# Optimization experiments

Measured on AMD Instinct MI355X. Metric: run time of the kernel, lower is better.

The kernel has to match this reference:

```python
import jax, jax.numpy as jnp
import numpy as np

N, D, E = 50000, 128, 800000
EPS_BN = 1e-5
EPS_NORM = 1e-12


def setup_inputs() -> dict:
    key = jax.random.key(0)
    ks = jax.random.split(key, 12)
    s = 1.0 / np.sqrt(D)  # xavier-ish scale for [D,D] weights
    return {
        "x": jax.random.normal(ks[0], (N, D), jnp.float32),
        "perb": jax.random.normal(ks[1], (N, D), jnp.float32) * 0.05,
        "edge_row": jax.random.randint(ks[2], (E,), 0, N, jnp.int32),
        "edge_col": jax.random.randint(ks[3], (E,), 0, N, jnp.int32),
        "edge_w": jax.random.uniform(ks[4], (E,), jnp.float32),
        "W_on": jax.random.normal(ks[5], (D, D), jnp.float32) * s,
        "b_on": jnp.zeros((D,), jnp.float32),
        "W_tg": jax.random.normal(ks[6], (D, D), jnp.float32) * s,
        "b_tg": jnp.zeros((D,), jnp.float32),
        "W1": jax.random.normal(ks[7], (D, D), jnp.float32) * s,
        "b1": jnp.zeros((D,), jnp.float32),
        "bn_g": jnp.ones((D,), jnp.float32),
        "bn_b": jnp.zeros((D,), jnp.float32),
        "prelu_a": jnp.full((1,), 0.25, jnp.float32),
        "W2": jax.random.normal(ks[8], (D, D), jnp.float32) * s,
        "b2": jnp.zeros((D,), jnp.float32),
    }


def _gcn(x, W, b, row, col, w):
    # dense matmul then sparse aggregation: out = A @ (x W) + b
    h = x @ W                              # [N, D]
    msg = h[col] * w[:, None]              # gather + edge weight, [E, D]
    agg = jax.ops.segment_sum(msg, row, num_segments=N)  # scatter-add, [N, D]
    return agg + b


def _predictor(x, W1, b1, g, beta, a, W2, b2):
    h = x @ W1 + b1
    mu = h.mean(axis=0)
    var = h.var(axis=0)  # biased, as torch BatchNorm1d normalization
    h = (h - mu) / jnp.sqrt(var + EPS_BN) * g + beta
    h = jnp.where(h > 0, h, a * h)  # PReLU (single shared slope)
    return h @ W2 + b2


def _l2norm(x):
    n = jnp.sqrt(jnp.sum(x * x, axis=-1, keepdims=True))
    return x / jnp.maximum(n, EPS_NORM)


def _loss_fn(x, y):
    return 2.0 - 2.0 * jnp.sum(_l2norm(x) * _l2norm(y), axis=-1)


def reference(x, perb, edge_row, edge_col, edge_w,
              W_on, b_on, W_tg, b_tg,
              W1, b1, bn_g, bn_b, prelu_a, W2, b2):
    x2 = x + perb
    embed = x2 + _gcn(x2, W_on, b_on, edge_row, edge_col, edge_w)
    online_x = _gcn(x, W_on, b_on, edge_row, edge_col, edge_w)
    online_y = _gcn(x2, W_on, b_on, edge_row, edge_col, edge_w)
    target_y = jax.lax.stop_gradient(_gcn(x, W_tg, b_tg, edge_row, edge_col, edge_w))
    target_x = jax.lax.stop_gradient(_gcn(x2, W_tg, b_tg, edge_row, edge_col, edge_w))
    px = _predictor(online_x, W1, b1, bn_g, bn_b, prelu_a, W2, b2)
    py = _predictor(online_y, W1, b1, bn_g, bn_b, prelu_a, W2, b2)
    loss = (_loss_fn(px, target_x) + _loss_fn(py, target_y)).mean()
    return embed, loss
```

## Files before the change

### kernel.cpp

```cpp
#include <hip/hip_runtime.h>

typedef unsigned int u32;
typedef unsigned short u16;
typedef __attribute__((ext_vector_type(8))) short short8;
typedef __attribute__((ext_vector_type(4))) float floatx4;

union F8 { uint4 u4; short8 s8; };

#define CAP 64
#define CSTR 16

__device__ __forceinline__ float bf2f(u32 lo16) { return __uint_as_float(lo16 << 16); }
__device__ __forceinline__ u16 f2bf(float f) {
    u32 u = __float_as_uint(f);
    return (u16)((u + 0x7FFFu + ((u >> 16) & 1u)) >> 16);
}
__device__ __forceinline__ u32 pack2(float a, float b) {
    return (u32)f2bf(a) | ((u32)f2bf(b) << 16);
}

__global__ __launch_bounds__(256) void k_front(
    const float* __restrict__ x, const float* __restrict__ perb,
    const int* __restrict__ erow, const int* __restrict__ ecol, const float* __restrict__ ew,
    const float* __restrict__ Won, const float* __restrict__ Wtg,
    const float* __restrict__ W1, const float* __restrict__ W2,
    const float* __restrict__ b_on, const float* __restrict__ b1,
    u16* __restrict__ XS, int* __restrict__ cnt, u32* __restrict__ cpack,
    u16* __restrict__ Wfrag, float* __restrict__ c1,
    int N, int E, int NC, int NS)
{
    int b = blockIdx.x, t = threadIdx.x;
    if (b < 8) {
        int s = (b << 8) + t;
        int lane = s & 63;
        int n = ((s >> 8) << 4) + (lane & 15);
        int k0 = ((s >> 6) & 3) * 32 + (lane >> 4) * 8;
        float v[8];
#pragma unroll
        for (int jj = 0; jj < 8; jj++) v[jj] = 0.f;
        for (int m2 = 0; m2 < 128; m2++) {
            float w1v = W1[m2 * 128 + n];
#pragma unroll
            for (int jj = 0; jj < 8; jj++)
                v[jj] = fmaf(Won[(k0 + jj) * 128 + m2], w1v, v[jj]);
        }
        ((uint4*)(Wfrag + 2 * 16384))[s] =
            make_uint4(pack2(v[0], v[1]), pack2(v[2], v[3]), pack2(v[4], v[5]), pack2(v[6], v[7]));
    } else if (b == 8) {
        if (t < 128) {
            float s = b1[t];
            for (int k = 0; k < 128; k++) s = fmaf(b_on[k], W1[k * 128 + t], s);
            c1[t] = s;
        }
    } else if (b < 12) {
        const float* W = (b == 9) ? Won : (b == 10 ? Wtg : W2);
        int mi = (b == 9) ? 0 : (b == 10 ? 1 : 3);
        uint4* out = (uint4*)(Wfrag + (size_t)mi * 16384);
        for (int s = t; s < 2048; s += 256) {
            int lane = s & 63;
            int n = ((s >> 8) << 4) + (lane & 15);
            int k0 = ((s >> 6) & 3) * 32 + (lane >> 4) * 8;
            u32 p[4];
#pragma unroll
            for (int jj = 0; jj < 4; jj++) {
                float a = W[(size_t)(k0 + 2 * jj) * 128 + n];
                float bb = W[(size_t)(k0 + 2 * jj + 1) * 128 + n];
                p[jj] = pack2(a, bb);
            }
            out[s] = make_uint4(p[0], p[1], p[2], p[3]);
        }
    } else {
        int t2 = b - 12;
        int T = NC + NS;
        int sc_before = (int)(((long long)t2 * NC) / T);
        int sc_after  = (int)(((long long)(t2 + 1) * NC) / T);
        if (sc_after > sc_before) {
            int e = sc_before * 256 + t;
            if (e < E) {
                int r = erow[e];
                u32 wq = (u32)__float2uint_rn(ew[e] * 65536.f);
                if (wq > 65535u) wq = 65535u;
                u32 rec = (u32)ecol[e] | (wq << 16);
                int tk = atomicAdd(&cnt[r * CSTR], 1);
                if (tk < CAP) cpack[(size_t)r * CAP + tk] = rec;
            }
        } else {
            int tid = (t2 - sc_before) * 256 + t;
            if (tid < N * 32) {
                int row = tid >> 5, seg = tid & 31;
                float4 xv = *(const float4*)(x + (size_t)row * 128 + seg * 4);
                float4 pv = *(const float4*)(perb + (size_t)row * 128 + seg * 4);
                u16* r = XS + (size_t)row * 256 + seg * 4;
                *(uint2*)r = make_uint2(pack2(xv.x, xv.y), pack2(xv.z, xv.w));
                *(uint2*)(r + 128) = make_uint2(pack2(xv.x + pv.x, xv.y + pv.y), pack2(xv.z + pv.z, xv.w + pv.w));
            }
        }
    }
}

__global__ __launch_bounds__(256) void k_agg(
    const u16* __restrict__ XS, const int* __restrict__ cnt,
    const u32* __restrict__ cpack, u16* __restrict__ AG, int N)
{
    int wave = threadIdx.x >> 6, lane = threadIdx.x & 63;
    int node = blockIdx.x * 4 + wave;
    if (node >= N) return;
    int d = cnt[node * CSTR];
    if (d > CAP) d = CAP;
    const u32* seg = cpack + (size_t)node * CAP;
    float a0 = 0.f, a1 = 0.f, a2 = 0.f, a3 = 0.f;
#pragma unroll 4
    for (int e = 0; e < d; e++) {
        u32 rec = seg[e];
        int c = (int)(rec & 0xffffu);
        float w = (float)(rec >> 16) * (1.f / 65536.f);
        uint2 v = ((const uint2*)(XS + (size_t)c * 256))[lane];
        a0 = fmaf(w, bf2f(v.x & 0xffffu), a0);
        a1 = fmaf(w, bf2f(v.x >> 16), a1);
        a2 = fmaf(w, bf2f(v.y & 0xffffu), a2);
        a3 = fmaf(w, bf2f(v.y >> 16), a3);
    }
    ((uint2*)(AG + (size_t)node * 256))[lane] = make_uint2(pack2(a0, a1), pack2(a2, a3));
}

__global__ __launch_bounds__(512) void k_hemb(
    const u16* __restrict__ AG, const u16* __restrict__ Wfrag,
    const float* __restrict__ c1, const float* __restrict__ b_on,
    const u16* __restrict__ XS,
    u16* __restrict__ h1x, u16* __restrict__ h1y, float* __restrict__ out,
    int N, int ntiles)
{
    __shared__ uint4 sW[4096];
    const int wave = threadIdx.x >> 6, lane = threadIdx.x & 63;
    const int m = lane & 15, q = lane >> 4;
    const uint4* wfWon = (const uint4*)Wfrag;
    const uint4* wfWc  = (const uint4*)(Wfrag + 2 * 16384);
#pragma unroll
    for (int i = threadIdx.x; i < 2048; i += 512) {
        sW[i]        = wfWon[i];
        sW[i + 2048] = wfWc[i];
    }
    __syncthreads();
    for (int tile = blockIdx.x; tile < ntiles; tile += gridDim.x) {
        const int grow = tile * 128 + wave * 16 + m;
        const int rc = grow < N ? grow : N - 1;
        const bool valid = grow < N;
        const u16* ar = AG + (size_t)rc * 256;
        short8 fa[4], fb[4];
#pragma unroll
        for (int ks = 0; ks < 4; ks++) {
            int c0 = ks * 32 + q * 8;
            F8 t;
            t.u4 = *(const uint4*)(ar + c0);       fa[ks] = t.s8;
            t.u4 = *(const uint4*)(ar + 128 + c0); fb[ks] = t.s8;
        }
#pragma unroll 2
        for (int ct = 0; ct < 8; ct++) {
            floatx4 ax = {0.f, 0.f, 0.f, 0.f}, ay = {0.f, 0.f, 0.f, 0.f}, em = {0.f, 0.f, 0.f, 0.f};
#pragma unroll
            for (int ks = 0; ks < 4; ks++) {
                F8 wc, wo;
                wo.u4 = sW[(ct * 4 + ks) * 64 + lane];
                wc.u4 = sW[2048 + (ct * 4 + ks) * 64 + lane];
                ax = __builtin_amdgcn_mfma_f32_16x16x32_bf16(wc.s8, fa[ks], ax, 0, 0, 0);
                ay = __builtin_amdgcn_mfma_f32_16x16x32_bf16(wc.s8, fb[ks], ay, 0, 0, 0);
                em = __builtin_amdgcn_mfma_f32_16x16x32_bf16(wo.s8, fb[ks], em, 0, 0, 0);
            }
            if (valid) {
                int c0 = ct * 16 + q * 4;
                float4 cv = *(const float4*)(c1 + c0);
                float4 bo = *(const float4*)(b_on + c0);
                uint2 xs2 = *(const uint2*)(XS + (size_t)grow * 256 + 128 + c0);
                *(uint2*)(h1x + (size_t)grow * 128 + c0) =
                    make_uint2(pack2(ax[0] + cv.x, ax[1] + cv.y), pack2(ax[2] + cv.z, ax[3] + cv.w));
                *(uint2*)(h1y + (size_t)grow * 128 + c0) =
                    make_uint2(pack2(ay[0] + cv.x, ay[1] + cv.y), pack2(ay[2] + cv.z, ay[3] + cv.w));
                float4 o;
                o.x = bf2f(xs2.x & 0xffffu) + em[0] + bo.x;
                o.y = bf2f(xs2.x >> 16)     + em[1] + bo.y;
                o.z = bf2f(xs2.y & 0xffffu) + em[2] + bo.z;
                o.w = bf2f(xs2.y >> 16)     + em[3] + bo.w;
                *(float4*)(out + (size_t)grow * 128 + c0) = o;
            }
        }
    }
}

__global__ __launch_bounds__(256) void k_bnstats(
    const u32* __restrict__ h1x32, const u32* __restrict__ h1y32,
    float* __restrict__ sums, int* __restrict__ tick,
    const float* __restrict__ g, const float* __restrict__ beta,
    float* __restrict__ bnp, int N)
{
    int c2 = threadIdx.x & 63, gg = threadIdx.x >> 6;
    int per = (N + gridDim.x - 1) / gridDim.x;
    int r0 = blockIdx.x * per, r1 = r0 + per;
    if (r1 > N) r1 = N;
    float s[8] = {0.f, 0.f, 0.f, 0.f, 0.f, 0.f, 0.f, 0.f};
    for (int r = r0 + gg; r < r1; r += 4) {
        u32 vx = h1x32[(size_t)r * 64 + c2];
        float lo = bf2f(vx & 0xffffu), hi = bf2f(vx >> 16);
        s[0] += lo; s[1] = fmaf(lo, lo, s[1]); s[2] += hi; s[3] = fmaf(hi, hi, s[3]);
        u32 vy = h1y32[(size_t)r * 64 + c2];
        lo = bf2f(vy & 0xffffu); hi = bf2f(vy >> 16);
        s[4] += lo; s[5] = fmaf(lo, lo, s[5]); s[6] += hi; s[7] = fmaf(hi, hi, s[7]);
    }
    __shared__ float red[256][8];
    __shared__ int lastflag;
#pragma unroll
    for (int k = 0; k < 8; k++) red[threadIdx.x][k] = s[k];
    __syncthreads();
    if (gg == 0) {
        float v[8];
#pragma unroll
        for (int k = 0; k < 8; k++)
            v[k] = red[c2][k] + red[c2 + 64][k] + red[c2 + 128][k] + red[c2 + 192][k];
        int c0 = 2 * c2, c1i = c0 + 1;
        atomicAdd(&sums[c0], v[0]);        atomicAdd(&sums[128 + c0], v[1]);
        atomicAdd(&sums[c1i], v[2]);       atomicAdd(&sums[128 + c1i], v[3]);
        atomicAdd(&sums[256 + c0], v[4]);  atomicAdd(&sums[384 + c0], v[5]);
        atomicAdd(&sums[256 + c1i], v[6]); atomicAdd(&sums[384 + c1i], v[7]);
    }
    __syncthreads();
    if (threadIdx.x == 0) {
        __threadfence();
        int old = atomicAdd(tick, 1);
        lastflag = (old == (int)gridDim.x - 1) ? 1 : 0;
    }
    __syncthreads();
    if (lastflag && threadIdx.x < 128) {
        int d = threadIdx.x;
        float inv = 1.0f / (float)N;
        float s0 = atomicAdd(&sums[d], 0.f);
        float s1 = atomicAdd(&sums[128 + d], 0.f);
        float s2 = atomicAdd(&sums[256 + d], 0.f);
        float s3 = atomicAdd(&sums[384 + d], 0.f);
        float mux = s0 * inv;
        float varx = s1 * inv - mux * mux;
        float isx = rsqrtf(varx + 1e-5f);
        bnp[d]       = g[d] * isx;
        bnp[128 + d] = beta[d] - mux * g[d] * isx;
        float muy = s2 * inv;
        float vary = s3 * inv - muy * muy;
        float isy = rsqrtf(vary + 1e-5f);
        bnp[256 + d] = g[d] * isy;
        bnp[384 + d] = beta[d] - muy * g[d] * isy;
    }
}

__device__ __forceinline__ short8 bn_frag(const u16* hrow, const float* sc, const float* sh,
                                          int c0, float slope) {
    uint4 h = *(const uint4*)(hrow + c0);
    float4 s0 = *(const float4*)(sc + c0), s1 = *(const float4*)(sc + c0 + 4);
    float4 t0 = *(const float4*)(sh + c0), t1 = *(const float4*)(sh + c0 + 4);
    float v[8];
    v[0] = fmaf(bf2f(h.x & 0xffffu), s0.x, t0.x);
    v[1] = fmaf(bf2f(h.x >> 16),     s0.y, t0.y);
    v[2] = fmaf(bf2f(h.y & 0xffffu), s0.z, t0.z);
    v[3] = fmaf(bf2f(h.y >> 16),     s0.w, t0.w);
    v[4] = fmaf(bf2f(h.z & 0xffffu), s1.x, t1.x);
    v[5] = fmaf(bf2f(h.z >> 16),     s1.y, t1.y);
    v[6] = fmaf(bf2f(h.w & 0xffffu), s1.z, t1.z);
    v[7] = fmaf(bf2f(h.w >> 16),     s1.w, t1.w);
#pragma unroll
    for (int j = 0; j < 8; j++) v[j] = v[j] > 0.f ? v[j] : slope * v[j];
    F8 r;
    r.u4 = make_uint4(pack2(v[0], v[1]), pack2(v[2], v[3]), pack2(v[4], v[5]), pack2(v[6], v[7]));
    return r.s8;
}

__global__ __launch_bounds__(512) void k_loss(
    const u16* __restrict__ h1x, const u16* __restrict__ h1y,
    const u16* __restrict__ AG, const u16* __restrict__ Wfrag,
    const float* __restrict__ bnp, const float* __restrict__ prelu_a,
    const float* __restrict__ b2, const float* __restrict__ b_tg,
    float* __restrict__ loss, int* __restrict__ tick, float* __restrict__ out,
    int N, int ntiles)
{
    __shared__ uint4 sW[4096];
    __shared__ float lred[8];
    __shared__ int lastflag;
    const int wave = threadIdx.x >> 6, lane = threadIdx.x & 63;
    const int m = lane & 15, q = lane >> 4;
    const float slope = prelu_a[0];
    const uint4* wfTg = (const uint4*)(Wfrag + 1 * 16384);
    const uint4* wfW2 = (const uint4*)(Wfrag + 3 * 16384);
#pragma unroll
    for (int i = threadIdx.x; i < 2048; i += 512) {
        sW[i]        = wfTg[i];
        sW[i + 2048] = wfW2[i];
    }
    __syncthreads();
    float lacc = 0.f;
    for (int tile = blockIdx.x; tile < ntiles; tile += gridDim.x) {
        const int grow = tile * 128 + wave * 16 + m;
        const int rc = grow < N ? grow : N - 1;
        const bool valid = grow < N;
        const u16* hx = h1x + (size_t)rc * 128;
        const u16* hy = h1y + (size_t)rc * 128;
        const u16* ar = AG + (size_t)rc * 256;
        short8 px8[4], py8[4], gx[4], gx2[4];
#pragma unroll
        for (int ks = 0; ks < 4; ks++) {
            int c0 = ks * 32 + q * 8;
            px8[ks] = bn_frag(hx, bnp, bnp + 128, c0, slope);
            py8[ks] = bn_frag(hy, bnp + 256, bnp + 384, c0, slope);
            F8 t;
            t.u4 = *(const uint4*)(ar + c0);       gx[ks] = t.s8;
            t.u4 = *(const uint4*)(ar + 128 + c0); gx2[ks] = t.s8;
        }
        float pp = 0.f, pt = 0.f, tt = 0.f, qq = 0.f, qs = 0.f, ss = 0.f;
#pragma unroll 2
        for (int ct = 0; ct < 8; ct++) {
            floatx4 ax = {0.f, 0.f, 0.f, 0.f}, ay = {0.f, 0.f, 0.f, 0.f};
            floatx4 atx = {0.f, 0.f, 0.f, 0.f}, aty = {0.f, 0.f, 0.f, 0.f};
#pragma unroll
            for (int ks = 0; ks < 4; ks++) {
                F8 w2, wt;
                wt.u4 = sW[(ct * 4 + ks) * 64 + lane];
                w2.u4 = sW[2048 + (ct * 4 + ks) * 64 + lane];
                ax  = __builtin_amdgcn_mfma_f32_16x16x32_bf16(w2.s8, px8[ks], ax, 0, 0, 0);
                ay  = __builtin_amdgcn_mfma_f32_16x16x32_bf16(w2.s8, py8[ks], ay, 0, 0, 0);
                atx = __builtin_amdgcn_mfma_f32_16x16x32_bf16(wt.s8, gx2[ks], atx, 0, 0, 0);
                aty = __builtin_amdgcn_mfma_f32_16x16x32_bf16(wt.s8, gx[ks], aty, 0, 0, 0);
            }
            int c0 = ct * 16 + q * 4;
            float4 bv = *(const float4*)(b2 + c0);
            float4 tb = *(const float4*)(b_tg + c0);
#pragma unroll
            for (int j = 0; j < 4; j++) {
                float bvj = j == 0 ? bv.x : (j == 1 ? bv.y : (j == 2 ? bv.z : bv.w));
                float tbj = j == 0 ? tb.x : (j == 1 ? tb.y : (j == 2 ? tb.z : tb.w));
                float pxv = ax[j] + bvj, txv = atx[j] + tbj;
                float pyv = ay[j] + bvj, tyv = aty[j] + tbj;
                pp = fmaf(pxv, pxv, pp); pt = fmaf(pxv, txv, pt); tt = fmaf(txv, txv, tt);
                qq = fmaf(pyv, pyv, qq); qs = fmaf(pyv, tyv, qs); ss = fmaf(tyv, tyv, ss);
            }
        }
        pp += __shfl_xor(pp, 16); pt += __shfl_xor(pt, 16); tt += __shfl_xor(tt, 16);
        qq += __shfl_xor(qq, 16); qs += __shfl_xor(qs, 16); ss += __shfl_xor(ss, 16);
        pp += __shfl_xor(pp, 32); pt += __shfl_xor(pt, 32); tt += __shfl_xor(tt, 32);
        qq += __shfl_xor(qq, 32); qs += __shfl_xor(qs, 32); ss += __shfl_xor(ss, 32);
        float cx = pt / (fmaxf(sqrtf(pp), 1e-12f) * fmaxf(sqrtf(tt), 1e-12f));
        float cy = qs / (fmaxf(sqrtf(qq), 1e-12f) * fmaxf(sqrtf(ss), 1e-12f));
        lacc += valid ? (4.f - 2.f * cx - 2.f * cy) : 0.f;
    }
    lacc += __shfl_xor(lacc, 1); lacc += __shfl_xor(lacc, 2);
    lacc += __shfl_xor(lacc, 4); lacc += __shfl_xor(lacc, 8);
    if (lane == 0) lred[wave] = lacc;
    __syncthreads();
    if (threadIdx.x == 0) {
        float bs = lred[0] + lred[1] + lred[2] + lred[3]
                 + lred[4] + lred[5] + lred[6] + lred[7];
        atomicAdd(loss, bs);
        __threadfence();
        int old = atomicAdd(tick, 1);
        lastflag = (old == (int)gridDim.x - 1) ? 1 : 0;
        if (lastflag) {
            float v = atomicAdd(loss, 0.f);
            out[(size_t)N * 128] = v * (1.0f / (float)N);
        }
    }
}

extern "C" void kernel_launch(void* const* d_in, const int* in_sizes, int n_in,
                              void* d_out, int out_size, void* d_ws, size_t ws_size,
                              hipStream_t stream)
{
    const float* x    = (const float*)d_in[0];
    const float* perb = (const float*)d_in[1];
    const int*   erow = (const int*)d_in[2];
    const int*   ecol = (const int*)d_in[3];
    const float* ew   = (const float*)d_in[4];
    const float* Won  = (const float*)d_in[5];
    const float* bon  = (const float*)d_in[6];
    const float* Wtg  = (const float*)d_in[7];
    const float* btg  = (const float*)d_in[8];
    const float* W1   = (const float*)d_in[9];
    const float* b1   = (const float*)d_in[10];
    const float* bng  = (const float*)d_in[11];
    const float* bnb  = (const float*)d_in[12];
    const float* pra  = (const float*)d_in[13];
    const float* W2   = (const float*)d_in[14];
    const float* b2   = (const float*)d_in[15];
    float* out = (float*)d_out;

    const int N = in_sizes[0] / 128;
    const int E = in_sizes[2];

    char* ws = (char*)d_ws;
    u16* XS  = (u16*)ws;
    u16* AG  = (u16*)(ws + (size_t)N * 512);
    u16* h1x = (u16*)(ws + (size_t)N * 1024);
    u16* h1y = (u16*)(ws + (size_t)N * 1024 + (size_t)N * 256);
    u32* cpack = (u32*)(ws + (size_t)N * 1024);

    char* p = ws + (size_t)N * 1024 + (size_t)N * 512;
    const size_t szcnt = (((size_t)N * CSTR * 4) + 63) & ~(size_t)63;
    int* cnt  = (int*)p;      p += szcnt;
    float* sums = (float*)p;  p += 2048;
    float* loss = (float*)p;  p += 64;
    int* ticks = (int*)p;     p += 64;
    size_t zero_bytes = (size_t)(p - (char*)cnt);
    float* c1 = (float*)p;    p += 512;
    float* bnp = (float*)p;   p += 2048;
    u16* Wfrag = (u16*)p;     p += 4 * 16384 * 2;

    hipMemsetAsync(cnt, 0, zero_bytes, stream);

    const int NS = (N * 32 + 255) / 256;
    const int NC = (E + 255) / 256;
    const int nt128 = (N + 127) / 128;

    k_front<<<12 + NC + NS, 256, 0, stream>>>(x, perb, erow, ecol, ew, Won, Wtg, W1, W2,
                                              bon, b1, XS, cnt, cpack, Wfrag, c1, N, E, NC, NS);
    k_agg<<<(N + 3) / 4, 256, 0, stream>>>(XS, cnt, cpack, AG, N);
    k_hemb<<<nt128, 512, 0, stream>>>(AG, Wfrag, c1, bon, XS, h1x, h1y, out, N, nt128);
    k_bnstats<<<256, 256, 0, stream>>>((const u32*)h1x, (const u32*)h1y, sums, ticks, bng, bnb, bnp, N);
    k_loss<<<nt128, 512, 0, stream>>>(h1x, h1y, AG, Wfrag, bnp, pra, b2, btg, loss, ticks + 1, out, N, nt128);
}
```

Baseline: 304.7 us.

## Fuse BatchNorm statistics reduction into the hemb MFMA kernel epilogue

Removes the separate k_bnstats kernel. The hemb kernel now reduces per-column sum and sum-of-squares of h1x/h1y with wave shuffles and pushes them into global sums with atomics, and the last block finalizes the BN parameters. This saves one launch and a full re-read of h1x/h1y from memory. In exchange it issues many more global float atomics onto only 512 addresses (one set per 16-row group per column tile), which can contend. The stats are also now taken from the fp32 values before bf16 rounding, which changes numerics slightly.

```diff
diff --git a/kernel.cpp b/kernel.cpp
--- a/kernel.cpp
+++ b/kernel.cpp
@@ -128,9 +128,13 @@
     const float* __restrict__ c1, const float* __restrict__ b_on,
     const u16* __restrict__ XS,
     u16* __restrict__ h1x, u16* __restrict__ h1y, float* __restrict__ out,
+    float* __restrict__ sums, int* __restrict__ tick,
+    const float* __restrict__ g, const float* __restrict__ beta,
+    float* __restrict__ bnp,
     int N, int ntiles)
 {
     __shared__ uint4 sW[4096];
+    __shared__ int lastflag;
     const int wave = threadIdx.x >> 6, lane = threadIdx.x & 63;
     const int m = lane & 15, q = lane >> 4;
     const uint4* wfWon = (const uint4*)Wfrag;
@@ -166,15 +170,22 @@
                 ay = __builtin_amdgcn_mfma_f32_16x16x32_bf16(wc.s8, fb[ks], ay, 0, 0, 0);
                 em = __builtin_amdgcn_mfma_f32_16x16x32_bf16(wo.s8, fb[ks], em, 0, 0, 0);
             }
+            int c0 = ct * 16 + q * 4;
+            float4 cv = *(const float4*)(c1 + c0);
+            float hx[4], hy[4];
+#pragma unroll
+            for (int j = 0; j < 4; j++) {
+                float cvj = j == 0 ? cv.x : (j == 1 ? cv.y : (j == 2 ? cv.z : cv.w));
+                hx[j] = ax[j] + cvj;
+                hy[j] = ay[j] + cvj;
+            }
             if (valid) {
-                int c0 = ct * 16 + q * 4;
-                float4 cv = *(const float4*)(c1 + c0);
                 float4 bo = *(const float4*)(b_on + c0);
                 uint2 xs2 = *(const uint2*)(XS + (size_t)grow * 256 + 128 + c0);
                 *(uint2*)(h1x + (size_t)grow * 128 + c0) =
-                    make_uint2(pack2(ax[0] + cv.x, ax[1] + cv.y), pack2(ax[2] + cv.z, ax[3] + cv.w));
+                    make_uint2(pack2(hx[0], hx[1]), pack2(hx[2], hx[3]));
                 *(uint2*)(h1y + (size_t)grow * 128 + c0) =
-                    make_uint2(pack2(ay[0] + cv.x, ay[1] + cv.y), pack2(ay[2] + cv.z, ay[3] + cv.w));
+                    make_uint2(pack2(hy[0], hy[1]), pack2(hy[2], hy[3]));
                 float4 o;
                 o.x = bf2f(xs2.x & 0xffffu) + em[0] + bo.x;
                 o.y = bf2f(xs2.x >> 16)     + em[1] + bo.y;
@@ -182,44 +193,34 @@
                 o.w = bf2f(xs2.y >> 16)     + em[3] + bo.w;
                 *(float4*)(out + (size_t)grow * 128 + c0) = o;
             }
-        }
-    }
-}
-
-__global__ __launch_bounds__(256) void k_bnstats(
-    const u32* __restrict__ h1x32, const u32* __restrict__ h1y32,
-    float* __restrict__ sums, int* __restrict__ tick,
-    const float* __restrict__ g, const float* __restrict__ beta,
-    float* __restrict__ bnp, int N)
-{
-    int c2 = threadIdx.x & 63, gg = threadIdx.x >> 6;
-    int per = (N + gridDim.x - 1) / gridDim.x;
-    int r0 = blockIdx.x * per, r1 = r0 + per;
-    if (r1 > N) r1 = N;
-    float s[8] = {0.f, 0.f, 0.f, 0.f, 0.f, 0.f, 0.f, 0.f};
-    for (int r = r0 + gg; r < r1; r += 4) {
-        u32 vx = h1x32[(size_t)r * 64 + c2];
-        float lo = bf2f(vx & 0xffffu), hi = bf2f(vx >> 16);
-        s[0] += lo; s[1] = fmaf(lo, lo, s[1]); s[2] += hi; s[3] = fmaf(hi, hi, s[3]);
-        u32 vy = h1y32[(size_t)r * 64 + c2];
-        lo = bf2f(vy & 0xffffu); hi = bf2f(vy >> 16);
-        s[4] += lo; s[5] = fmaf(lo, lo, s[5]); s[6] += hi; s[7] = fmaf(hi, hi, s[7]);
-    }
-    __shared__ float red[256][8];
-    __shared__ int lastflag;
-#pragma unroll
-    for (int k = 0; k < 8; k++) red[threadIdx.x][k] = s[k];
-    __syncthreads();
-    if (gg == 0) {
-        float v[8];
-#pragma unroll
-        for (int k = 0; k < 8; k++)
-            v[k] = red[c2][k] + red[c2 + 64][k] + red[c2 + 128][k] + red[c2 + 192][k];
-        int c0 = 2 * c2, c1i = c0 + 1;
-        atomicAdd(&sums[c0], v[0]);        atomicAdd(&sums[128 + c0], v[1]);
-        atomicAdd(&sums[c1i], v[2]);       atomicAdd(&sums[128 + c1i], v[3]);
-        atomicAdd(&sums[256 + c0], v[4]);  atomicAdd(&sums[384 + c0], v[5]);
-        atomicAdd(&sums[256 + c1i], v[6]); atomicAdd(&sums[384 + c1i], v[7]);
+            float sx[4], sxx[4], sy[4], syy[4];
+#pragma unroll
+            for (int j = 0; j < 4; j++) {
+                float vx = valid ? hx[j] : 0.f;
+                float vy = valid ? hy[j] : 0.f;
+                sx[j] = vx;  sxx[j] = vx * vx;
+                sy[j] = vy;  syy[j] = vy * vy;
+            }
+#pragma unroll
+            for (int r = 1; r < 16; r <<= 1) {
+#pragma unroll
+                for (int j = 0; j < 4; j++) {
+                    sx[j]  += __shfl_xor(sx[j],  r);
+                    sxx[j] += __shfl_xor(sxx[j], r);
+                    sy[j]  += __shfl_xor(sy[j],  r);
+                    syy[j] += __shfl_xor(syy[j], r);
+                }
+            }
+            if (m == 0) {
+#pragma unroll
+                for (int j = 0; j < 4; j++) {
+                    atomicAdd(&sums[c0 + j],       sx[j]);
+                    atomicAdd(&sums[128 + c0 + j], sxx[j]);
+                    atomicAdd(&sums[256 + c0 + j], sy[j]);
+                    atomicAdd(&sums[384 + c0 + j], syy[j]);
+                }
+            }
+        }
     }
     __syncthreads();
     if (threadIdx.x == 0) {
@@ -415,7 +416,7 @@
     k_front<<<12 + NC + NS, 256, 0, stream>>>(x, perb, erow, ecol, ew, Won, Wtg, W1, W2,
                                               bon, b1, XS, cnt, cpack, Wfrag, c1, N, E, NC, NS);
     k_agg<<<(N + 3) / 4, 256, 0, stream>>>(XS, cnt, cpack, AG, N);
-    k_hemb<<<nt128, 512, 0, stream>>>(AG, Wfrag, c1, bon, XS, h1x, h1y, out, N, nt128);
-    k_bnstats<<<256, 256, 0, stream>>>((const u32*)h1x, (const u32*)h1y, sums, ticks, bng, bnb, bnp, N);
+    k_hemb<<<nt128, 512, 0, stream>>>(AG, Wfrag, c1, bon, XS, h1x, h1y, out,
+                                      sums, ticks, bng, bnb, bnp, N, nt128);
     k_loss<<<nt128, 512, 0, stream>>>(h1x, h1y, AG, Wfrag, bnp, pra, b2, btg, loss, ticks + 1, out, N, nt128);
 }
```

New measurement: 686.5 us. 2.25x slower.
